# Kernel tuning notes

Measured on AMD Instinct MI355X. Metric: run time of the kernel, lower is better.

## Reference

```python
import jax, jax.numpy as jnp
import numpy as np

N_GRAPHS = 256
NODES_PER_GRAPH = 64
N_NODES = N_GRAPHS * NODES_PER_GRAPH  # 16384
IN_F = 128
OUT_F = 128
N_HEADS = 16


def setup_inputs() -> dict:
    key = jax.random.key(0)
    k1, k2, k3, k4 = jax.random.split(key, 4)
    inputs = jax.random.normal(k1, (N_NODES, IN_F), dtype=jnp.float32)
    # fixed equal-sized graphs so sum(n_node) == N_NODES exactly
    n_node = jnp.full((N_GRAPHS,), NODES_PER_GRAPH, dtype=jnp.int32)
    head = jax.random.randint(k2, (N_GRAPHS,), 0, N_HEADS, dtype=jnp.int32)
    # lecun_normal-like init: std = 1/sqrt(fan_in)
    kernel = jax.random.normal(k3, (N_HEADS, IN_F, OUT_F), dtype=jnp.float32) * (1.0 / np.sqrt(IN_F))
    bias = jax.random.normal(k4, (N_HEADS, OUT_F), dtype=jnp.float32) * 0.02
    return {"inputs": inputs, "n_node": n_node, "head": head, "kernel": kernel, "bias": bias}


def reference(inputs, n_node, head, kernel, bias):
    # per-node head index: repeat each graph's head over its nodes
    node_head = jnp.repeat(head, n_node, total_repeat_length=inputs.shape[0])  # [N]
    k = kernel[node_head]                       # [N, in, out] (gathered per-node weights)
    y = jnp.einsum('bi,bio->bo', inputs, k)     # [N, out]
    y = y + bias[node_head]                     # [N, out]
    return y
```

## Files before the change

### kernel.cpp

```cpp
#include <hip/hip_runtime.h>
#include <hip/hip_bf16.h>

#define NG   256
#define NPG  64
#define INF  128
#define OUTF 128
#define NH   16

#define LDSK 136

typedef __attribute__((ext_vector_type(8))) short bf16x8;
typedef __attribute__((ext_vector_type(4))) float f32x4;

__device__ __forceinline__ ushort f2bf(float f) {
    union { float f; unsigned int i; } c; c.f = f;
    unsigned int r = c.i + 0x7fffu + ((c.i >> 16) & 1u);
    return (ushort)(r >> 16);
}

__global__ __launch_bounds__(512) void mhl_fused_kernel(
    const float* __restrict__ X,
    const int*   __restrict__ head,
    const float* __restrict__ W,
    const float* __restrict__ bias,
    float*       __restrict__ Y)
{
    __shared__ ushort Wl[OUTF * LDSK];

    int g = (int)blockIdx.x;
    int h = head[g];
    int t = (int)threadIdx.x;

    {
        int k  = t >> 2;
        int c0 = (t & 3) * 32;
        const float* src = W + h * (INF * OUTF) + k * OUTF + c0;
#pragma unroll
        for (int j = 0; j < 32; j += 4) {
            float4 v = *(const float4*)(src + j);
            Wl[(c0 + j + 0) * LDSK + k] = f2bf(v.x);
            Wl[(c0 + j + 1) * LDSK + k] = f2bf(v.y);
            Wl[(c0 + j + 2) * LDSK + k] = f2bf(v.z);
            Wl[(c0 + j + 3) * LDSK + k] = f2bf(v.w);
        }
    }
    __syncthreads();

    int wave = t >> 6;
    int lane = t & 63;
    int quad = lane >> 4;
    int l16  = lane & 15;

    int mrow = (wave & 3) * 16;
    int ncol = (wave >> 2) * 64;

    const float* Xg = X + (g * NPG + mrow + l16) * INF + quad * 8;
    bf16x8 a[4];
#pragma unroll
    for (int kt = 0; kt < 4; ++kt) {
        float v[8] __attribute__((aligned(16)));
        *(float4*)(&v[0]) = *(const float4*)(Xg + kt * 32);
        *(float4*)(&v[4]) = *(const float4*)(Xg + kt * 32 + 4);
#pragma unroll
        for (int j = 0; j < 8; ++j) a[kt][j] = (short)f2bf(v[j]);
    }

    f32x4 acc[4];
#pragma unroll
    for (int nt = 0; nt < 4; ++nt) acc[nt] = (f32x4){0.f, 0.f, 0.f, 0.f};

#pragma unroll
    for (int nt = 0; nt < 4; ++nt) {
        const ushort* Wn = &Wl[(ncol + nt * 16 + l16) * LDSK + quad * 8];
#pragma unroll
        for (int kt = 0; kt < 4; ++kt) {
            bf16x8 b = *(const bf16x8*)(Wn + kt * 32);
            acc[nt] = __builtin_amdgcn_mfma_f32_16x16x32_bf16(a[kt], b, acc[nt], 0, 0, 0);
        }
    }

    float* Yg = Y + (g * NPG + mrow) * OUTF + ncol;
#pragma unroll
    for (int nt = 0; nt < 4; ++nt) {
        float bv = bias[h * OUTF + ncol + nt * 16 + l16];
#pragma unroll
        for (int r = 0; r < 4; ++r)
            Yg[(quad * 4 + r) * OUTF + nt * 16 + l16] = acc[nt][r] + bv;
    }
}

extern "C" void kernel_launch(void* const* d_in, const int* in_sizes, int n_in,
                              void* d_out, int out_size, void* d_ws, size_t ws_size,
                              hipStream_t stream) {
    const float* X    = (const float*)d_in[0];
    const int*   head = (const int*)d_in[2];
    const float* W    = (const float*)d_in[3];
    const float* bias = (const float*)d_in[4];
    float* Y = (float*)d_out;

    mhl_fused_kernel<<<NG, 512, 0, stream>>>(X, head, W, bias, Y);
}
```

Before: 71.17 us.

## Pre-convert per-head weights to transposed bf16 once, load fragments directly

Adds a pre-pass kernel that converts all 16 head weight matrices to transposed bf16 in workspace, so the GEMM kernel no longer reconverts and LDS-stages its head's weights in every one of 256 blocks. The GEMM kernel loads B fragments straight from global/L2 into registers, drops the shared-memory barrier, and uses nontemporal stores for the output. In exchange it adds a second kernel launch and a dependency between the two kernels, and register pressure from holding 16 B fragments. It falls back to the fused kernel when no workspace is available.

```diff
diff --git a/kernel.cpp b/kernel.cpp
--- a/kernel.cpp
+++ b/kernel.cpp
@@ -10,27 +10,114 @@
 #define LDSK 136
 
 typedef __attribute__((ext_vector_type(8))) short bf16x8;
+typedef __attribute__((ext_vector_type(8))) unsigned short u16x8;
 typedef __attribute__((ext_vector_type(4))) float f32x4;
 
-__device__ __forceinline__ ushort f2bf(float f) {
+__device__ __forceinline__ unsigned short f2bf(float f) {
     union { float f; unsigned int i; } c; c.f = f;
     unsigned int r = c.i + 0x7fffu + ((c.i >> 16) & 1u);
-    return (ushort)(r >> 16);
+    return (unsigned short)(r >> 16);
+}
+
+__global__ __launch_bounds__(256) void wconv_kernel(
+    const float* __restrict__ W, unsigned short* __restrict__ Wt)
+{
+    __shared__ unsigned short T[16 * LDSK];
+    int b  = (int)blockIdx.x;
+    int h  = b >> 3;
+    int n0 = (b & 7) * 16;
+    int t  = (int)threadIdx.x;
+    const float* Wh = W + h * (INF * OUTF);
+#pragma unroll
+    for (int i = 0; i < 2; ++i) {
+        int flat = i * 256 + t;
+        int k = flat >> 2;
+        int c = (flat & 3) * 4;
+        float4 v = *(const float4*)(Wh + k * OUTF + n0 + c);
+        T[(c + 0) * LDSK + k] = f2bf(v.x);
+        T[(c + 1) * LDSK + k] = f2bf(v.y);
+        T[(c + 2) * LDSK + k] = f2bf(v.z);
+        T[(c + 3) * LDSK + k] = f2bf(v.w);
+    }
+    __syncthreads();
+    int n  = t >> 4;
+    int kc = t & 15;
+    u16x8 r = *(const u16x8*)(&T[n * LDSK + kc * 8]);
+    *(u16x8*)(Wt + h * (OUTF * INF) + (n0 + n) * INF + kc * 8) = r;
+}
+
+__global__ __launch_bounds__(512) void mhl_gemm_kernel(
+    const float* __restrict__ X,
+    const int*   __restrict__ head,
+    const unsigned short* __restrict__ Wt,
+    const float* __restrict__ bias,
+    float*       __restrict__ Y)
+{
+    int g = (int)blockIdx.x;
+    int h = head[g];
+    int t = (int)threadIdx.x;
+    int wave = t >> 6, lane = t & 63;
+    int quad = lane >> 4, l16 = lane & 15;
+    int mrow = (wave & 3) * 16;
+    int ncol = (wave >> 2) * 64;
+
+    const float* Xg = X + (g * NPG + mrow + l16) * INF + quad * 8;
+    float4 xv[8];
+#pragma unroll
+    for (int kt = 0; kt < 4; ++kt) {
+        xv[2 * kt]     = *(const float4*)(Xg + kt * 32);
+        xv[2 * kt + 1] = *(const float4*)(Xg + kt * 32 + 4);
+    }
+
+    const unsigned short* Wb = Wt + h * (OUTF * INF) + quad * 8;
+    bf16x8 bfrag[4][4];
+#pragma unroll
+    for (int nt = 0; nt < 4; ++nt) {
+        const unsigned short* Wn = Wb + (ncol + nt * 16 + l16) * INF;
+#pragma unroll
+        for (int kt = 0; kt < 4; ++kt)
+            bfrag[nt][kt] = *(const bf16x8*)(Wn + kt * 32);
+    }
+
+    bf16x8 a[4];
+#pragma unroll
+    for (int kt = 0; kt < 4; ++kt) {
+        float vv[8] __attribute__((aligned(16)));
+        *(float4*)(&vv[0]) = xv[2 * kt];
+        *(float4*)(&vv[4]) = xv[2 * kt + 1];
+#pragma unroll
+        for (int j = 0; j < 8; ++j) a[kt][j] = (short)f2bf(vv[j]);
+    }
+
+    f32x4 acc[4];
+#pragma unroll
+    for (int nt = 0; nt < 4; ++nt) acc[nt] = (f32x4){0.f, 0.f, 0.f, 0.f};
+#pragma unroll
+    for (int nt = 0; nt < 4; ++nt)
+#pragma unroll
+        for (int kt = 0; kt < 4; ++kt)
+            acc[nt] = __builtin_amdgcn_mfma_f32_16x16x32_bf16(a[kt], bfrag[nt][kt], acc[nt], 0, 0, 0);
+
+    float* Yg = Y + (g * NPG + mrow) * OUTF + ncol;
+#pragma unroll
+    for (int nt = 0; nt < 4; ++nt) {
+        float bv = bias[h * OUTF + ncol + nt * 16 + l16];
+#pragma unroll
+        for (int r = 0; r < 4; ++r)
+            __builtin_nontemporal_store(acc[nt][r] + bv,
+                &Yg[(quad * 4 + r) * OUTF + nt * 16 + l16]);
+    }
 }
 
 __global__ __launch_bounds__(512) void mhl_fused_kernel(
-    const float* __restrict__ X,
-    const int*   __restrict__ head,
-    const float* __restrict__ W,
-    const float* __restrict__ bias,
-    float*       __restrict__ Y)
+    const float* __restrict__ X, const int* __restrict__ head,
+    const float* __restrict__ W, const float* __restrict__ bias,
+    float* __restrict__ Y)
 {
-    __shared__ ushort Wl[OUTF * LDSK];
-
+    __shared__ unsigned short Wl[OUTF * LDSK];
     int g = (int)blockIdx.x;
     int h = head[g];
     int t = (int)threadIdx.x;
-
     {
         int k  = t >> 2;
         int c0 = (t & 3) * 32;
@@ -45,15 +132,10 @@
         }
     }
     __syncthreads();
-
-    int wave = t >> 6;
-    int lane = t & 63;
-    int quad = lane >> 4;
-    int l16  = lane & 15;
-
+    int wave = t >> 6, lane = t & 63;
+    int quad = lane >> 4, l16 = lane & 15;
     int mrow = (wave & 3) * 16;
     int ncol = (wave >> 2) * 64;
-
     const float* Xg = X + (g * NPG + mrow + l16) * INF + quad * 8;
     bf16x8 a[4];
 #pragma unroll
@@ -64,21 +146,18 @@
 #pragma unroll
         for (int j = 0; j < 8; ++j) a[kt][j] = (short)f2bf(v[j]);
     }
-
     f32x4 acc[4];
 #pragma unroll
     for (int nt = 0; nt < 4; ++nt) acc[nt] = (f32x4){0.f, 0.f, 0.f, 0.f};
-
 #pragma unroll
     for (int nt = 0; nt < 4; ++nt) {
-        const ushort* Wn = &Wl[(ncol + nt * 16 + l16) * LDSK + quad * 8];
+        const unsigned short* Wn = &Wl[(ncol + nt * 16 + l16) * LDSK + quad * 8];
 #pragma unroll
         for (int kt = 0; kt < 4; ++kt) {
-            bf16x8 b = *(const bf16x8*)(Wn + kt * 32);
-            acc[nt] = __builtin_amdgcn_mfma_f32_16x16x32_bf16(a[kt], b, acc[nt], 0, 0, 0);
+            bf16x8 bv = *(const bf16x8*)(Wn + kt * 32);
+            acc[nt] = __builtin_amdgcn_mfma_f32_16x16x32_bf16(a[kt], bv, acc[nt], 0, 0, 0);
         }
     }
-
     float* Yg = Y + (g * NPG + mrow) * OUTF + ncol;
 #pragma unroll
     for (int nt = 0; nt < 4; ++nt) {
@@ -98,5 +177,12 @@
     const float* bias = (const float*)d_in[4];
     float* Y = (float*)d_out;
 
-    mhl_fused_kernel<<<NG, 512, 0, stream>>>(X, head, W, bias, Y);
+    const size_t wt_bytes = (size_t)NH * OUTF * INF * sizeof(unsigned short);
+    if (d_ws != nullptr && ws_size >= wt_bytes) {
+        unsigned short* Wt = (unsigned short*)d_ws;
+        wconv_kernel<<<NH * 8, 256, 0, stream>>>(W, Wt);
+        mhl_gemm_kernel<<<NG, 512, 0, stream>>>(X, head, Wt, bias, Y);
+    } else {
+        mhl_fused_kernel<<<NG, 512, 0, stream>>>(X, head, W, bias, Y);
+    }
 }
```

Result: slower. 74.63 us (+4.9%).

## Prefetch X before weight staging, vectorize transposed LDS weight stores, nontemporal output

Applied to the files above, without the earlier changes.

The X rows are now loaded into registers before the weight fetch, and bias loads are hoisted ahead of the barrier, so global latencies overlap. Weight staging is rewritten so each thread reads float2 pairs across 8 k rows and writes two 16-byte bf16x8 vectors into the transposed LDS layout, replacing many scalar 2-byte LDS stores. Output stores become nontemporal to avoid polluting cache. In exchange, register pressure rises and the strided float2 global reads of W are less coalesced.

```diff
diff --git a/kernel.cpp b/kernel.cpp
--- a/kernel.cpp
+++ b/kernel.cpp
@@ -1,5 +1,4 @@
 #include <hip/hip_runtime.h>
-#include <hip/hip_bf16.h>
 
 #define NG   256
 #define NPG  64
@@ -12,10 +11,10 @@
 typedef __attribute__((ext_vector_type(8))) short bf16x8;
 typedef __attribute__((ext_vector_type(4))) float f32x4;
 
-__device__ __forceinline__ ushort f2bf(float f) {
+__device__ __forceinline__ unsigned short f2bf(float f) {
     union { float f; unsigned int i; } c; c.f = f;
     unsigned int r = c.i + 0x7fffu + ((c.i >> 16) & 1u);
-    return (ushort)(r >> 16);
+    return (unsigned short)(r >> 16);
 }
 
 __global__ __launch_bounds__(512) void mhl_fused_kernel(
@@ -25,44 +24,62 @@
     const float* __restrict__ bias,
     float*       __restrict__ Y)
 {
-    __shared__ ushort Wl[OUTF * LDSK];
+    __shared__ __align__(16) unsigned short Wl[OUTF * LDSK];
 
     int g = (int)blockIdx.x;
-    int h = head[g];
     int t = (int)threadIdx.x;
-
-    {
-        int k  = t >> 2;
-        int c0 = (t & 3) * 32;
-        const float* src = W + h * (INF * OUTF) + k * OUTF + c0;
-#pragma unroll
-        for (int j = 0; j < 32; j += 4) {
-            float4 v = *(const float4*)(src + j);
-            Wl[(c0 + j + 0) * LDSK + k] = f2bf(v.x);
-            Wl[(c0 + j + 1) * LDSK + k] = f2bf(v.y);
-            Wl[(c0 + j + 2) * LDSK + k] = f2bf(v.z);
-            Wl[(c0 + j + 3) * LDSK + k] = f2bf(v.w);
-        }
-    }
-    __syncthreads();
-
-    int wave = t >> 6;
-    int lane = t & 63;
-    int quad = lane >> 4;
-    int l16  = lane & 15;
-
+    int wave = t >> 6, lane = t & 63;
+    int quad = lane >> 4, l16 = lane & 15;
     int mrow = (wave & 3) * 16;
     int ncol = (wave >> 2) * 64;
 
     const float* Xg = X + (g * NPG + mrow + l16) * INF + quad * 8;
+    float4 xv[8];
+#pragma unroll
+    for (int kt = 0; kt < 4; ++kt) {
+        xv[2 * kt]     = *(const float4*)(Xg + kt * 32);
+        xv[2 * kt + 1] = *(const float4*)(Xg + kt * 32 + 4);
+    }
+
+    int h = head[g];
+
+    {
+        const float* Wh = W + h * (INF * OUTF);
+#pragma unroll
+        for (int c = 0; c < 2; ++c) {
+            int idx = c * 512 + t;
+            int n0 = (idx & 63) * 2;
+            int k0 = (idx >> 6) * 8;
+            float2 v[8];
+#pragma unroll
+            for (int j = 0; j < 8; ++j)
+                v[j] = *(const float2*)(Wh + (k0 + j) * OUTF + n0);
+            bf16x8 a0, a1;
+#pragma unroll
+            for (int j = 0; j < 8; ++j) {
+                a0[j] = (short)f2bf(v[j].x);
+                a1[j] = (short)f2bf(v[j].y);
+            }
+            *(bf16x8*)(&Wl[(n0 + 0) * LDSK + k0]) = a0;
+            *(bf16x8*)(&Wl[(n0 + 1) * LDSK + k0]) = a1;
+        }
+    }
+
+    float bv[4];
+#pragma unroll
+    for (int nt = 0; nt < 4; ++nt)
+        bv[nt] = bias[h * OUTF + ncol + nt * 16 + l16];
+
+    __syncthreads();
+
     bf16x8 a[4];
 #pragma unroll
     for (int kt = 0; kt < 4; ++kt) {
-        float v[8] __attribute__((aligned(16)));
-        *(float4*)(&v[0]) = *(const float4*)(Xg + kt * 32);
-        *(float4*)(&v[4]) = *(const float4*)(Xg + kt * 32 + 4);
+        float vv[8] __attribute__((aligned(16)));
+        *(float4*)(&vv[0]) = xv[2 * kt];
+        *(float4*)(&vv[4]) = xv[2 * kt + 1];
 #pragma unroll
-        for (int j = 0; j < 8; ++j) a[kt][j] = (short)f2bf(v[j]);
+        for (int j = 0; j < 8; ++j) a[kt][j] = (short)f2bf(vv[j]);
     }
 
     f32x4 acc[4];
@@ -71,7 +88,7 @@
 
 #pragma unroll
     for (int nt = 0; nt < 4; ++nt) {
-        const ushort* Wn = &Wl[(ncol + nt * 16 + l16) * LDSK + quad * 8];
+        const unsigned short* Wn = &Wl[(ncol + nt * 16 + l16) * LDSK + quad * 8];
 #pragma unroll
         for (int kt = 0; kt < 4; ++kt) {
             bf16x8 b = *(const bf16x8*)(Wn + kt * 32);
@@ -82,10 +99,10 @@
     float* Yg = Y + (g * NPG + mrow) * OUTF + ncol;
 #pragma unroll
     for (int nt = 0; nt < 4; ++nt) {
-        float bv = bias[h * OUTF + ncol + nt * 16 + l16];
 #pragma unroll
         for (int r = 0; r < 4; ++r)
-            Yg[(quad * 4 + r) * OUTF + nt * 16 + l16] = acc[nt][r] + bv;
+            __builtin_nontemporal_store(acc[nt][r] + bv[nt],
+                &Yg[(quad * 4 + r) * OUTF + nt * 16 + l16]);
     }
 }
 
```

After: 69.68 us. -2.1%, faster.
